# Performance work log

Measured on AMD Instinct MI355X. Metric: run time of the kernel, lower is better.

The kernel has to match this reference:

```python
import jax, jax.numpy as jnp
import numpy as np
import math

FEATURE_DIM = 1024
NUM_HEADS = 16
HEAD_SIZE = FEATURE_DIM // NUM_HEADS


def setup_inputs() -> dict:
    key = jax.random.key(0)
    ks = jax.random.split(key, 5)
    B, T, C = 4, 2048, FEATURE_DIM
    scale = 1.0 / math.sqrt(C)
    x = jax.random.normal(ks[0], (B, T, C), dtype=jnp.float32)
    # attention_proj: Linear(C, 3C) -> weight (3C, C), bias (3C,)
    W_qkv = jax.random.uniform(ks[1], (3 * C, C), jnp.float32, -scale, scale)
    b_qkv = jax.random.uniform(ks[2], (3 * C,), jnp.float32, -scale, scale)
    # final_proj: Linear(C, C)
    W_out = jax.random.uniform(ks[3], (C, C), jnp.float32, -scale, scale)
    b_out = jax.random.uniform(ks[4], (C,), jnp.float32, -scale, scale)
    return {"x": x, "W_qkv": W_qkv, "b_qkv": b_qkv, "W_out": W_out, "b_out": b_out}


def reference(x, W_qkv, b_qkv, W_out, b_out):
    B, T, C = x.shape
    H, hs = NUM_HEADS, HEAD_SIZE
    qkv = x @ W_qkv.T + b_qkv                     # (B, T, 3C)
    qkv = qkv.reshape(B, T, H, 3 * hs)            # per-head interleaved q|k|v
    q = qkv[..., :hs]                             # (B, T, H, hs)
    k = qkv[..., hs:2 * hs]
    v = qkv[..., 2 * hs:]
    att = jnp.einsum('bthd,bshd->bhts', q, k) / math.sqrt(hs)  # (B, H, T, T)
    att_prob = jax.nn.softmax(att, axis=-1)
    att_v = jnp.einsum('bhts,bshd->bthd', att_prob, v)         # (B, T, H, hs)
    att_v = att_v.reshape(B, T, C)
    return att_v @ W_out.T + b_out
```

## Files before the change

### kernel.cpp

```cpp
#include <hip/hip_runtime.h>
#include <hip/hip_bf16.h>


typedef unsigned short u16;
typedef short bf16x8 __attribute__((ext_vector_type(8)));
typedef float floatx4 __attribute__((ext_vector_type(4)));

#define BB 4
#define TT 2048
#define CC 1024
#define HH 16

#if __has_builtin(__builtin_amdgcn_exp2f)
#define EXP2(x) __builtin_amdgcn_exp2f(x)
#else
#define EXP2(x) exp2f(x)
#endif

__device__ __forceinline__ u16 f2bf(float f) {
    __hip_bfloat16 h = __float2bfloat16(f);
    u16 r; __builtin_memcpy(&r, &h, 2); return r;
}
__device__ __forceinline__ unsigned pkbf(float lo, float hi) {
    __hip_bfloat162 h2 = __float22bfloat162_rn(float2{lo, hi});
    unsigned r; __builtin_memcpy(&r, &h2, 4); return r;
}
__device__ __forceinline__ bf16x8 cvt8(const float* p) {
    floatx4 a = *(const floatx4*)p;
    floatx4 b = *(const floatx4*)(p + 4);
    bf16x8 r;
    r[0] = (short)f2bf(a[0]); r[1] = (short)f2bf(a[1]);
    r[2] = (short)f2bf(a[2]); r[3] = (short)f2bf(a[3]);
    r[4] = (short)f2bf(b[0]); r[5] = (short)f2bf(b[1]);
    r[6] = (short)f2bf(b[2]); r[7] = (short)f2bf(b[3]);
    return r;
}
__device__ __forceinline__ int sw8(int row, int slot) {
    return row * 64 + (((slot ^ (row & 7)) & 7) << 3);
}
__device__ __forceinline__ void gll16(const u16* g, u16* l) {
    __builtin_amdgcn_global_load_lds(
        (const __attribute__((address_space(1))) unsigned*)g,
        (__attribute__((address_space(3))) unsigned*)l, 16, 0, 0);
}

__device__ __forceinline__ void pl32swap(unsigned& a, unsigned& b) {
#if __has_builtin(__builtin_amdgcn_permlane32_swap)
    typedef unsigned u32x2 __attribute__((ext_vector_type(2)));
    u32x2 r = __builtin_amdgcn_permlane32_swap(a, b, false, false);
    a = r[0]; b = r[1];
#else
    const bool up = (threadIdx.x & 32) != 0;
    unsigned as = (unsigned)__shfl_xor((int)a, 32);
    unsigned bs = (unsigned)__shfl_xor((int)b, 32);
    unsigned na = up ? bs : a;
    unsigned nb = up ? b : as;
    a = na; b = nb;
#endif
}
__device__ __forceinline__ void pl16swap(unsigned& a, unsigned& b) {
#if __has_builtin(__builtin_amdgcn_permlane16_swap)
    typedef unsigned u32x2 __attribute__((ext_vector_type(2)));
    u32x2 r = __builtin_amdgcn_permlane16_swap(a, b, false, false);
    a = r[0]; b = r[1];
#else
    const bool up = (threadIdx.x & 16) != 0;
    unsigned as = (unsigned)__shfl_xor((int)a, 16);
    unsigned bs = (unsigned)__shfl_xor((int)b, 16);
    unsigned na = up ? bs : a;
    unsigned nb = up ? b : as;
    a = na; b = nb;
#endif
}

__global__ __launch_bounds__(256) void cvt_all(const float* __restrict__ x,
                                               const float* __restrict__ wq,
                                               const float* __restrict__ wo,
                                               u16* __restrict__ xb,
                                               u16* __restrict__ wqb,
                                               u16* __restrict__ wob) {
    const int nx8 = 8388608 / 8, nq8 = 3145728 / 8, no8 = 1048576 / 8;
    const int n8 = nx8 + nq8 + no8;
    for (int i = blockIdx.x * blockDim.x + threadIdx.x; i < n8;
         i += gridDim.x * blockDim.x) {
        const float* src;
        u16* dst;
        if (i < nx8)            { src = x  + (size_t)i * 8;          dst = xb  + (size_t)i * 8; }
        else if (i < nx8 + nq8) { size_t j = i - nx8; src = wq + j * 8; dst = wqb + j * 8; }
        else                    { size_t j = i - nx8 - nq8; src = wo + j * 8; dst = wob + j * 8; }
        floatx4 a = *(const floatx4*)src;
        floatx4 b = *(const floatx4*)(src + 4);
        union { bf16x8 v; unsigned u[4]; } r;
        r.u[0] = pkbf(a[0], a[1]); r.u[1] = pkbf(a[2], a[3]);
        r.u[2] = pkbf(b[0], b[1]); r.u[3] = pkbf(b[2], b[3]);
        *(bf16x8*)dst = r.v;
    }
}

template <int SCATTER, int QSLOT>
__global__ __launch_bounds__(256) void gemm_lds(const u16* __restrict__ Ab,
                                                const u16* __restrict__ Bb,
                                                const float* __restrict__ bias,
                                                void* __restrict__ Cv,
                                                int K, int N) {
    __shared__ u16 As[128 * 64];
    __shared__ u16 Bs[128 * 64];

    const int tid  = threadIdx.x;
    const int lane = tid & 63;
    const int wave = tid >> 6;
    const int quad = lane >> 4;
    const int l15  = lane & 15;
    const int wm   = (wave >> 1) * 64;
    const int wn   = (wave & 1) * 64;
    const int blockM = blockIdx.y * 128;
    const int blockN = blockIdx.x * 128;

    floatx4 acc[4][4];
#pragma unroll
    for (int i = 0; i < 4; i++)
#pragma unroll
        for (int j = 0; j < 4; j++) acc[i][j] = (floatx4){0.f, 0.f, 0.f, 0.f};

    const int lr = lane >> 3;
    const int scol = ((lane & 7) ^ (lr & 7)) * 8;

    for (int k0 = 0; k0 < K; k0 += 64) {
        __syncthreads();
#pragma unroll
        for (int i = 0; i < 4; i++) {
            const int c = wave * 4 + i;
            const int row = blockM + c * 8 + lr;
            const u16* src;
            if (QSLOT) {
                const int b = row >> 11, t = row & 2047, h = k0 >> 6;
                src = Ab + ((size_t)((b * HH + h) * TT + t)) * 192 + scol;
            } else {
                src = Ab + (size_t)row * K + k0 + scol;
            }
            gll16(src, &As[c * 512]);
        }
#pragma unroll
        for (int i = 0; i < 4; i++) {
            const int c = wave * 4 + i;
            const int row = blockN + c * 8 + lr;
            gll16(Bb + (size_t)row * K + k0 + scol, &Bs[c * 512]);
        }
        __syncthreads();

#pragma unroll
        for (int ks = 0; ks < 2; ks++) {
            const int slot = ks * 4 + quad;
            bf16x8 af[4], bfr[4];
#pragma unroll
            for (int mi = 0; mi < 4; mi++)
                af[mi] = *(const bf16x8*)&As[sw8(wm + mi * 16 + l15, slot)];
#pragma unroll
            for (int ni = 0; ni < 4; ni++)
                bfr[ni] = *(const bf16x8*)&Bs[sw8(wn + ni * 16 + l15, slot)];
#pragma unroll
            for (int mi = 0; mi < 4; mi++)
#pragma unroll
                for (int ni = 0; ni < 4; ni++)
                    acc[mi][ni] = __builtin_amdgcn_mfma_f32_16x16x32_bf16(
                        af[mi], bfr[ni], acc[mi][ni], 0, 0, 0);
        }
    }

#pragma unroll
    for (int ni = 0; ni < 4; ni++) {
        const int col = blockN + wn + ni * 16 + l15;
        const float bv = bias[col];
        if (SCATTER) {
            const int h = col / 192;
            const int r = col - h * 192;
            u16* C = (u16*)Cv;
#pragma unroll
            for (int mi = 0; mi < 4; mi++)
#pragma unroll
                for (int reg = 0; reg < 4; reg++) {
                    const int row = blockM + wm + mi * 16 + quad * 4 + reg;
                    const int b = row >> 11, t = row & 2047;
                    C[((size_t)((b * HH + h) * TT + t)) * 192 + r] =
                        f2bf(acc[mi][ni][reg] + bv);
                }
        } else {
            float* C = (float*)Cv;
#pragma unroll
            for (int mi = 0; mi < 4; mi++)
#pragma unroll
                for (int reg = 0; reg < 4; reg++) {
                    const int row = blockM + wm + mi * 16 + quad * 4 + reg;
                    C[(size_t)row * N + col] = acc[mi][ni][reg] + bv;
                }
        }
    }
}

template <int SCATTER, int QSLOT>
__global__ __launch_bounds__(256) void gemm_bt(const void* __restrict__ Av,
                                               const float* __restrict__ Bw,
                                               const float* __restrict__ bias,
                                               void* __restrict__ Cv,
                                               int K, int N) {
    __shared__ u16 As[128 * 64];
    __shared__ u16 Bs[128 * 64];

    const int tid  = threadIdx.x;
    const int lane = tid & 63;
    const int wave = tid >> 6;
    const int quad = lane >> 4;
    const int l15  = lane & 15;
    const int wm   = (wave >> 1) * 64;
    const int wn   = (wave & 1) * 64;
    const int blockM = blockIdx.y * 128;
    const int blockN = blockIdx.x * 128;

    floatx4 acc[4][4];
#pragma unroll
    for (int i = 0; i < 4; i++)
#pragma unroll
        for (int j = 0; j < 4; j++) acc[i][j] = (floatx4){0.f, 0.f, 0.f, 0.f};

    const int srow = lane >> 3;
    const int scol = (lane & 7) * 8;

    for (int k0 = 0; k0 < K; k0 += 64) {
        bf16x8 at[4], bt[4];
#pragma unroll
        for (int i = 0; i < 4; i++) {
            const int row = blockM + (i * 4 + wave) * 8 + srow;
            if (QSLOT) {
                const int b = row >> 11, t = row & 2047, h = k0 >> 6;
                at[i] = *(const bf16x8*)((const u16*)Av
                         + ((size_t)((b * HH + h) * TT + t)) * 192 + scol);
            } else {
                at[i] = cvt8((const float*)Av + (size_t)row * K + k0 + scol);
            }
        }
#pragma unroll
        for (int i = 0; i < 4; i++)
            bt[i] = cvt8(Bw + (size_t)(blockN + (i * 4 + wave) * 8 + srow) * K + k0 + scol);

        __syncthreads();
#pragma unroll
        for (int i = 0; i < 4; i++)
            *(bf16x8*)&As[sw8((i * 4 + wave) * 8 + srow, lane & 7)] = at[i];
#pragma unroll
        for (int i = 0; i < 4; i++)
            *(bf16x8*)&Bs[sw8((i * 4 + wave) * 8 + srow, lane & 7)] = bt[i];
        __syncthreads();

#pragma unroll
        for (int ks = 0; ks < 2; ks++) {
            const int slot = ks * 4 + quad;
            bf16x8 af[4], bfr[4];
#pragma unroll
            for (int mi = 0; mi < 4; mi++)
                af[mi] = *(const bf16x8*)&As[sw8(wm + mi * 16 + l15, slot)];
#pragma unroll
            for (int ni = 0; ni < 4; ni++)
                bfr[ni] = *(const bf16x8*)&Bs[sw8(wn + ni * 16 + l15, slot)];
#pragma unroll
            for (int mi = 0; mi < 4; mi++)
#pragma unroll
                for (int ni = 0; ni < 4; ni++)
                    acc[mi][ni] = __builtin_amdgcn_mfma_f32_16x16x32_bf16(
                        af[mi], bfr[ni], acc[mi][ni], 0, 0, 0);
        }
    }

#pragma unroll
    for (int ni = 0; ni < 4; ni++) {
        const int col = blockN + wn + ni * 16 + l15;
        const float bv = bias[col];
        if (SCATTER) {
            const int h = col / 192;
            const int r = col - h * 192;
            u16* C = (u16*)Cv;
#pragma unroll
            for (int mi = 0; mi < 4; mi++)
#pragma unroll
                for (int reg = 0; reg < 4; reg++) {
                    const int row = blockM + wm + mi * 16 + quad * 4 + reg;
                    const int b = row >> 11, t = row & 2047;
                    C[((size_t)((b * HH + h) * TT + t)) * 192 + r] =
                        f2bf(acc[mi][ni][reg] + bv);
                }
        } else {
            float* C = (float*)Cv;
#pragma unroll
            for (int mi = 0; mi < 4; mi++)
#pragma unroll
                for (int reg = 0; reg < 4; reg++) {
                    const int row = blockM + wm + mi * 16 + quad * 4 + reg;
                    C[(size_t)row * N + col] = acc[mi][ni][reg] + bv;
                }
        }
    }
}

__global__ __launch_bounds__(256) void attn_fwd(u16* __restrict__ qkv) {
    __shared__ u16 Ks[64 * 64];
    __shared__ u16 Vts[64 * 64];

    const int tid  = threadIdx.x;
    const int lane = tid & 63;
    const int wave = tid >> 6;
    const int quad = lane >> 4;
    const int l15  = lane & 15;

    const int bh = blockIdx.y;
    const int t0 = blockIdx.x * 128;
    u16* Qg = qkv + (size_t)bh * TT * 192;

    bf16x8 qf[2][2];
#pragma unroll
    for (int qi = 0; qi < 2; qi++) {
        const int trow = t0 + wave * 32 + qi * 16 + l15;
#pragma unroll
        for (int ks = 0; ks < 2; ks++)
            qf[qi][ks] = *(const bf16x8*)(Qg + (size_t)trow * 192 + ks * 32 + quad * 8);
    }

    floatx4 o[2][4];
#pragma unroll
    for (int qi = 0; qi < 2; qi++)
#pragma unroll
        for (int di = 0; di < 4; di++) o[qi][di] = (floatx4){0.f, 0.f, 0.f, 0.f};
    float l_run[2] = {0.f, 0.f};

    const float cexp = 0.18033688f;
    const int srow = lane >> 3;
    const int scol = (lane & 7) * 8;
    const int vs   = lane;
    const int vd0  = wave * 16;

    for (int s0 = 0; s0 < TT; s0 += 64) {
        bf16x8 kt[2];
#pragma unroll
        for (int i = 0; i < 2; i++)
            kt[i] = *(const bf16x8*)(Qg + (size_t)(s0 + (i * 4 + wave) * 8 + srow) * 192
                                     + 64 + scol);
        const u16* vp = Qg + (size_t)(s0 + vs) * 192 + 128 + vd0;
        bf16x8 v0 = *(const bf16x8*)vp;
        bf16x8 v1 = *(const bf16x8*)(vp + 8);

        __syncthreads();
#pragma unroll
        for (int i = 0; i < 2; i++)
            *(bf16x8*)&Ks[sw8((i * 4 + wave) * 8 + srow, lane & 7)] = kt[i];
        {
            const int vslot = vs >> 3, voff = vs & 7;
#pragma unroll
            for (int j = 0; j < 8; j++) {
                const int row = vd0 + j;
                Vts[row * 64 + (((vslot ^ (row & 7)) & 7) << 3) + voff] = (u16)v0[j];
            }
#pragma unroll
            for (int j = 0; j < 8; j++) {
                const int row = vd0 + 8 + j;
                Vts[row * 64 + (((vslot ^ (row & 7)) & 7) << 3) + voff] = (u16)v1[j];
            }
        }
        __syncthreads();

        floatx4 s_acc[4][2];
#pragma unroll
        for (int si = 0; si < 4; si++)
#pragma unroll
            for (int qi = 0; qi < 2; qi++) s_acc[si][qi] = (floatx4){0.f, 0.f, 0.f, 0.f};
#pragma unroll
        for (int ks = 0; ks < 2; ks++) {
            const int slot = ks * 4 + quad;
            bf16x8 kf[4];
#pragma unroll
            for (int si = 0; si < 4; si++)
                kf[si] = *(const bf16x8*)&Ks[sw8(si * 16 + l15, slot)];
#pragma unroll
            for (int si = 0; si < 4; si++)
#pragma unroll
                for (int qi = 0; qi < 2; qi++)
                    s_acc[si][qi] = __builtin_amdgcn_mfma_f32_16x16x32_bf16(
                        kf[si], qf[qi][ks], s_acc[si][qi], 0, 0, 0);
        }

        unsigned c[4][2][2];
        floatx4 rs[2] = {(floatx4){0.f,0.f,0.f,0.f}, (floatx4){0.f,0.f,0.f,0.f}};
#pragma unroll
        for (int si = 0; si < 4; si++)
#pragma unroll
            for (int qi = 0; qi < 2; qi++) {
                floatx4 p;
#pragma unroll
                for (int r = 0; r < 4; r++) p[r] = EXP2(s_acc[si][qi][r] * cexp);
                rs[qi] += p;
                c[si][qi][0] = pkbf(p[0], p[1]);
                c[si][qi][1] = pkbf(p[2], p[3]);
            }
#pragma unroll
        for (int qi = 0; qi < 2; qi++) {
            float v = rs[qi][0] + rs[qi][1] + rs[qi][2] + rs[qi][3];
            v += __shfl_xor(v, 16);
            v += __shfl_xor(v, 32);
            l_run[qi] += v;
        }

        union PF { bf16x8 v; unsigned u[4]; } pf[2][2];
#pragma unroll
        for (int qi = 0; qi < 2; qi++)
#pragma unroll
            for (int ks = 0; ks < 2; ks++)
#pragma unroll
                for (int h = 0; h < 2; h++) {
                    unsigned a = c[2 * ks][qi][h];
                    unsigned b = c[2 * ks + 1][qi][h];
                    pl32swap(a, b);
                    pl16swap(a, b);
                    pf[qi][ks].u[h]     = a;
                    pf[qi][ks].u[2 + h] = b;
                }

#pragma unroll
        for (int ks = 0; ks < 2; ks++) {
            const int slot = ks * 4 + quad;
            bf16x8 vf[4];
#pragma unroll
            for (int di = 0; di < 4; di++)
                vf[di] = *(const bf16x8*)&Vts[sw8(di * 16 + l15, slot)];
#pragma unroll
            for (int qi = 0; qi < 2; qi++)
#pragma unroll
                for (int di = 0; di < 4; di++)
                    o[qi][di] = __builtin_amdgcn_mfma_f32_16x16x32_bf16(
                        pf[qi][ks].v, vf[di], o[qi][di], 0, 0, 0);
        }
    }

#pragma unroll
    for (int qi = 0; qi < 2; qi++)
#pragma unroll
        for (int reg = 0; reg < 4; reg++) {
            const float lv = __shfl(l_run[qi], quad * 4 + reg);
            const float inv_l = 1.0f / lv;
            const int trow = t0 + wave * 32 + qi * 16 + quad * 4 + reg;
#pragma unroll
            for (int di = 0; di < 4; di++)
                Qg[(size_t)trow * 192 + di * 16 + l15] = f2bf(o[qi][di][reg] * inv_l);
        }
}

extern "C" void kernel_launch(void* const* d_in, const int* in_sizes, int n_in,
                              void* d_out, int out_size, void* d_ws, size_t ws_size,
                              hipStream_t stream) {
    (void)out_size;
    float* out = (float*)d_out;

    const float *x = nullptr, *wq = nullptr, *bq = nullptr, *wo = nullptr, *bo = nullptr;
    int found = 0;
    for (int i = 0; i < n_in && i < 8; i++) {
        switch (in_sizes[i]) {
            case 8388608: x  = (const float*)d_in[i]; found |= 1;  break;
            case 3145728: wq = (const float*)d_in[i]; found |= 2;  break;
            case 3072:    bq = (const float*)d_in[i]; found |= 4;  break;
            case 1048576: wo = (const float*)d_in[i]; found |= 8;  break;
            case 1024:    bo = (const float*)d_in[i]; found |= 16; break;
        }
    }
    if (found != 31) {
        x  = (const float*)d_in[0]; wq = (const float*)d_in[1];
        bq = (const float*)d_in[2]; wo = (const float*)d_in[3];
        bo = (const float*)d_in[4];
    }

    u16* qkv = (u16*)d_ws;

    if (ws_size >= 75497472u) {
        u16* xb  = qkv + 25165824;
        u16* wqb = qkv + 33554432;
        u16* wob = qkv + 36700160;

        cvt_all<<<2048, 256, 0, stream>>>(x, wq, wo, xb, wqb, wob);
        gemm_lds<1, 0><<<dim3(3 * CC / 128, BB * TT / 128), 256, 0, stream>>>(
            xb, wqb, bq, qkv, CC, 3 * CC);
        attn_fwd<<<dim3(TT / 128, BB * HH), 256, 0, stream>>>(qkv);
        gemm_lds<0, 1><<<dim3(CC / 128, BB * TT / 128), 256, 0, stream>>>(
            qkv, wob, bo, out, CC, CC);
    } else {
        gemm_bt<1, 0><<<dim3(3 * CC / 128, BB * TT / 128), 256, 0, stream>>>(
            x, wq, bq, qkv, CC, 3 * CC);
        attn_fwd<<<dim3(TT / 128, BB * HH), 256, 0, stream>>>(qkv);
        gemm_bt<0, 1><<<dim3(CC / 128, BB * TT / 128), 256, 0, stream>>>(
            qkv, wo, bo, out, CC, CC);
    }
}
```

Before: 304.6 us.

## Pre-transpose V into separate buffer, load K/V via direct-to-LDS, remap GEMM tiles

Adds a transpose_v kernel that writes V in a (bh, d, t) layout so the attention kernel can fill its K and V LDS tiles with direct global-to-LDS 16-byte loads. This replaces the per-element scattered transposing stores into LDS. The GEMM kernels also remap workgroup IDs in groups of 8 so that neighbouring workgroups are spread across the grid, intended to improve cache locality across XCDs. The cost is one extra kernel launch and an extra read and write of V, plus a larger workspace requirement, with the old path kept as a fallback.

Result: slower. 330.8 us (+8.6%).

```diff
diff --git a/kernel.cpp b/kernel.cpp
--- a/kernel.cpp
+++ b/kernel.cpp
@@ -97,6 +97,41 @@
     }
 }
 
+__global__ __launch_bounds__(256) void transpose_v(const u16* __restrict__ qkv,
+                                                   u16* __restrict__ Vt) {
+    __shared__ u16 L[128 * 64];
+    const int tid = threadIdx.x;
+    const int bh  = blockIdx.y;
+    const int t0  = blockIdx.x * 128;
+    const u16* Vg = qkv + (size_t)bh * TT * 192 + 128;
+
+    const int lr = tid >> 3;
+    const int p8 = tid & 7;
+#pragma unroll
+    for (int p = 0; p < 4; p++) {
+        const int t = p * 32 + lr;
+        bf16x8 v = *(const bf16x8*)(Vg + (size_t)(t0 + t) * 192 + p8 * 8);
+        *(bf16x8*)&L[sw8(t, p8)] = v;
+    }
+    __syncthreads();
+
+    const int tseg = (tid & 15) * 8;
+    const int dq   = tid >> 4;
+#pragma unroll
+    for (int p = 0; p < 4; p++) {
+        const int d = p * 16 + dq;
+        const int slot = d >> 3, off = d & 7;
+        union { bf16x8 v; u16 e[8]; } r;
+#pragma unroll
+        for (int j = 0; j < 8; j++) {
+            const int jj = (j + tid) & 7;
+            const int t = tseg + jj;
+            r.e[jj] = L[t * 64 + (((slot ^ (t & 7)) & 7) << 3) + off];
+        }
+        *(bf16x8*)(Vt + ((size_t)bh * 64 + d) * TT + t0 + tseg) = r.v;
+    }
+}
+
 template <int SCATTER, int QSLOT>
 __global__ __launch_bounds__(256) void gemm_lds(const u16* __restrict__ Ab,
                                                 const u16* __restrict__ Bb,
@@ -113,8 +148,12 @@
     const int l15  = lane & 15;
     const int wm   = (wave >> 1) * 64;
     const int wn   = (wave & 1) * 64;
-    const int blockM = blockIdx.y * 128;
-    const int blockN = blockIdx.x * 128;
+
+    const int gx = gridDim.x, nwg = gx * gridDim.y;
+    int id = blockIdx.y * gx + blockIdx.x;
+    if ((nwg & 7) == 0) id = (id & 7) * (nwg >> 3) + (id >> 3);
+    const int blockM = (id / gx) * 128;
+    const int blockN = (id % gx) * 128;
 
     floatx4 acc[4][4];
 #pragma unroll
@@ -300,7 +339,9 @@
     }
 }
 
-__global__ __launch_bounds__(256) void attn_fwd(u16* __restrict__ qkv) {
+template <int VT>
+__global__ __launch_bounds__(256) void attn_fwd(u16* __restrict__ qkv,
+                                                const u16* __restrict__ Vt) {
     __shared__ u16 Ks[64 * 64];
     __shared__ u16 Vts[64 * 64];
 
@@ -313,6 +354,7 @@
     const int bh = blockIdx.y;
     const int t0 = blockIdx.x * 128;
     u16* Qg = qkv + (size_t)bh * TT * 192;
+    const u16* VtB = Vt + (size_t)bh * 64 * TT;
 
     bf16x8 qf[2][2];
 #pragma unroll
@@ -331,39 +373,57 @@
     float l_run[2] = {0.f, 0.f};
 
     const float cexp = 0.18033688f;
-    const int srow = lane >> 3;
-    const int scol = (lane & 7) * 8;
+    const int lr   = lane >> 3;
+    const int scolsw = ((lane & 7) ^ (lr & 7)) * 8;
+    const int scol   = (lane & 7) * 8;
     const int vs   = lane;
     const int vd0  = wave * 16;
 
     for (int s0 = 0; s0 < TT; s0 += 64) {
-        bf16x8 kt[2];
-#pragma unroll
-        for (int i = 0; i < 2; i++)
-            kt[i] = *(const bf16x8*)(Qg + (size_t)(s0 + (i * 4 + wave) * 8 + srow) * 192
-                                     + 64 + scol);
-        const u16* vp = Qg + (size_t)(s0 + vs) * 192 + 128 + vd0;
-        bf16x8 v0 = *(const bf16x8*)vp;
-        bf16x8 v1 = *(const bf16x8*)(vp + 8);
-
-        __syncthreads();
-#pragma unroll
-        for (int i = 0; i < 2; i++)
-            *(bf16x8*)&Ks[sw8((i * 4 + wave) * 8 + srow, lane & 7)] = kt[i];
-        {
-            const int vslot = vs >> 3, voff = vs & 7;
-#pragma unroll
-            for (int j = 0; j < 8; j++) {
-                const int row = vd0 + j;
-                Vts[row * 64 + (((vslot ^ (row & 7)) & 7) << 3) + voff] = (u16)v0[j];
+        if (VT) {
+            __syncthreads();
+#pragma unroll
+            for (int i = 0; i < 2; i++) {
+                const int c = wave * 2 + i;
+                gll16(Qg + (size_t)(s0 + c * 8 + lr) * 192 + 64 + scolsw,
+                      &Ks[c * 512]);
             }
 #pragma unroll
-            for (int j = 0; j < 8; j++) {
-                const int row = vd0 + 8 + j;
-                Vts[row * 64 + (((vslot ^ (row & 7)) & 7) << 3) + voff] = (u16)v1[j];
+            for (int i = 0; i < 2; i++) {
+                const int c = wave * 2 + i;
+                gll16(VtB + (size_t)(c * 8 + lr) * TT + s0 + scolsw,
+                      &Vts[c * 512]);
             }
-        }
-        __syncthreads();
+            __syncthreads();
+        } else {
+            bf16x8 kt[2];
+#pragma unroll
+            for (int i = 0; i < 2; i++)
+                kt[i] = *(const bf16x8*)(Qg + (size_t)(s0 + (i * 4 + wave) * 8 + lr) * 192
+                                         + 64 + scol);
+            const u16* vp = Qg + (size_t)(s0 + vs) * 192 + 128 + vd0;
+            bf16x8 v0 = *(const bf16x8*)vp;
+            bf16x8 v1 = *(const bf16x8*)(vp + 8);
+
+            __syncthreads();
+#pragma unroll
+            for (int i = 0; i < 2; i++)
+                *(bf16x8*)&Ks[sw8((i * 4 + wave) * 8 + lr, lane & 7)] = kt[i];
+            {
+                const int vslot = vs >> 3, voff = vs & 7;
+#pragma unroll
+                for (int j = 0; j < 8; j++) {
+                    const int row = vd0 + j;
+                    Vts[row * 64 + (((vslot ^ (row & 7)) & 7) << 3) + voff] = (u16)v0[j];
+                }
+#pragma unroll
+                for (int j = 0; j < 8; j++) {
+                    const int row = vd0 + 8 + j;
+                    Vts[row * 64 + (((vslot ^ (row & 7)) & 7) << 3) + voff] = (u16)v1[j];
+                }
+            }
+            __syncthreads();
+        }
 
         floatx4 s_acc[4][2];
 #pragma unroll
@@ -475,22 +535,31 @@
 
     u16* qkv = (u16*)d_ws;
 
-    if (ws_size >= 75497472u) {
+    const dim3 g1(3 * CC / 128, BB * TT / 128), ga(TT / 128, BB * HH),
+               g3(CC / 128, BB * TT / 128);
+
+    if (ws_size >= 92274688u) {
         u16* xb  = qkv + 25165824;
         u16* wqb = qkv + 33554432;
         u16* wob = qkv + 36700160;
+        u16* Vt  = qkv + 37748736;
 
         cvt_all<<<2048, 256, 0, stream>>>(x, wq, wo, xb, wqb, wob);
-        gemm_lds<1, 0><<<dim3(3 * CC / 128, BB * TT / 128), 256, 0, stream>>>(
-            xb, wqb, bq, qkv, CC, 3 * CC);
-        attn_fwd<<<dim3(TT / 128, BB * HH), 256, 0, stream>>>(qkv);
-        gemm_lds<0, 1><<<dim3(CC / 128, BB * TT / 128), 256, 0, stream>>>(
-            qkv, wob, bo, out, CC, CC);
+        gemm_lds<1, 0><<<g1, 256, 0, stream>>>(xb, wqb, bq, qkv, CC, 3 * CC);
+        transpose_v<<<ga, 256, 0, stream>>>(qkv, Vt);
+        attn_fwd<1><<<ga, 256, 0, stream>>>(qkv, Vt);
+        gemm_lds<0, 1><<<g3, 256, 0, stream>>>(qkv, wob, bo, out, CC, CC);
+    } else if (ws_size >= 75497472u) {
+        u16* xb  = qkv + 25165824;
+        u16* wqb = qkv + 33554432;
+        u16* wob = qkv + 36700160;
+        cvt_all<<<2048, 256, 0, stream>>>(x, wq, wo, xb, wqb, wob);
+        gemm_lds<1, 0><<<g1, 256, 0, stream>>>(xb, wqb, bq, qkv, CC, 3 * CC);
+        attn_fwd<0><<<ga, 256, 0, stream>>>(qkv, nullptr);
+        gemm_lds<0, 1><<<g3, 256, 0, stream>>>(qkv, wob, bo, out, CC, CC);
     } else {
-        gemm_bt<1, 0><<<dim3(3 * CC / 128, BB * TT / 128), 256, 0, stream>>>(
-            x, wq, bq, qkv, CC, 3 * CC);
-        attn_fwd<<<dim3(TT / 128, BB * HH), 256, 0, stream>>>(qkv);
-        gemm_bt<0, 1><<<dim3(CC / 128, BB * TT / 128), 256, 0, stream>>>(
-            qkv, wo, bo, out, CC, CC);
-    }
-}
+        gemm_bt<1, 0><<<g1, 256, 0, stream>>>(x, wq, bq, qkv, CC, 3 * CC);
+        attn_fwd<0><<<ga, 256, 0, stream>>>(qkv, nullptr);
+        gemm_bt<0, 1><<<g3, 256, 0, stream>>>(qkv, wo, bo, out, CC, CC);
+    }
+}
```

## Fold softmax scale into Q, compute row sums via MFMA, async-load K to LDS

Applied to the files above, without the earlier changes.

The QKV GEMM epilogue now premultiplies Q columns by the log2-scaled softmax factor, so the attention loop drops the per-element multiply before exp2. The softmax row sum is accumulated with an extra MFMA against a vector of bf16 ones instead of VALU adds and cross-lane shuffles. K tiles are loaded with a direct global-to-LDS instruction (gll16) with pre-swizzled addresses instead of going through registers. In exchange, row sums are now taken from bf16-rounded probabilities, and Q is stored in bf16 after scaling, which slightly changes rounding. The kernel still runs without a running max.

Result: faster. 295.0 us (-3.2%).

```diff
diff --git a/kernel.cpp b/kernel.cpp
--- a/kernel.cpp
+++ b/kernel.cpp
@@ -10,6 +10,7 @@
 #define TT 2048
 #define CC 1024
 #define HH 16
+#define CEXP 0.18033688f
 
 #if __has_builtin(__builtin_amdgcn_exp2f)
 #define EXP2(x) __builtin_amdgcn_exp2f(x)
@@ -174,6 +175,7 @@
         if (SCATTER) {
             const int h = col / 192;
             const int r = col - h * 192;
+            const float qs = (r < 64) ? CEXP : 1.0f;
             u16* C = (u16*)Cv;
 #pragma unroll
             for (int mi = 0; mi < 4; mi++)
@@ -182,7 +184,7 @@
                     const int row = blockM + wm + mi * 16 + quad * 4 + reg;
                     const int b = row >> 11, t = row & 2047;
                     C[((size_t)((b * HH + h) * TT + t)) * 192 + r] =
-                        f2bf(acc[mi][ni][reg] + bv);
+                        f2bf((acc[mi][ni][reg] + bv) * qs);
                 }
         } else {
             float* C = (float*)Cv;
@@ -277,6 +279,7 @@
         if (SCATTER) {
             const int h = col / 192;
             const int r = col - h * 192;
+            const float qs = (r < 64) ? CEXP : 1.0f;
             u16* C = (u16*)Cv;
 #pragma unroll
             for (int mi = 0; mi < 4; mi++)
@@ -285,7 +288,7 @@
                     const int row = blockM + wm + mi * 16 + quad * 4 + reg;
                     const int b = row >> 11, t = row & 2047;
                     C[((size_t)((b * HH + h) * TT + t)) * 192 + r] =
-                        f2bf(acc[mi][ni][reg] + bv);
+                        f2bf((acc[mi][ni][reg] + bv) * qs);
                 }
         } else {
             float* C = (float*)Cv;
@@ -323,33 +326,33 @@
             qf[qi][ks] = *(const bf16x8*)(Qg + (size_t)trow * 192 + ks * 32 + quad * 8);
     }
 
+    bf16x8 ones;
+#pragma unroll
+    for (int j = 0; j < 8; j++) ones[j] = (short)0x3F80;
+
     floatx4 o[2][4];
 #pragma unroll
     for (int qi = 0; qi < 2; qi++)
 #pragma unroll
         for (int di = 0; di < 4; di++) o[qi][di] = (floatx4){0.f, 0.f, 0.f, 0.f};
-    float l_run[2] = {0.f, 0.f};
-
-    const float cexp = 0.18033688f;
-    const int srow = lane >> 3;
-    const int scol = (lane & 7) * 8;
+    floatx4 l_acc[2] = {(floatx4){0.f,0.f,0.f,0.f}, (floatx4){0.f,0.f,0.f,0.f}};
+
+    const int lr = lane >> 3;
+    const int scolsw = ((lane & 7) ^ (lr & 7)) * 8;
     const int vs   = lane;
     const int vd0  = wave * 16;
 
     for (int s0 = 0; s0 < TT; s0 += 64) {
-        bf16x8 kt[2];
-#pragma unroll
-        for (int i = 0; i < 2; i++)
-            kt[i] = *(const bf16x8*)(Qg + (size_t)(s0 + (i * 4 + wave) * 8 + srow) * 192
-                                     + 64 + scol);
         const u16* vp = Qg + (size_t)(s0 + vs) * 192 + 128 + vd0;
         bf16x8 v0 = *(const bf16x8*)vp;
         bf16x8 v1 = *(const bf16x8*)(vp + 8);
 
         __syncthreads();
 #pragma unroll
-        for (int i = 0; i < 2; i++)
-            *(bf16x8*)&Ks[sw8((i * 4 + wave) * 8 + srow, lane & 7)] = kt[i];
+        for (int i = 0; i < 2; i++) {
+            const int c = wave * 2 + i;
+            gll16(Qg + (size_t)(s0 + c * 8 + lr) * 192 + 64 + scolsw, &Ks[c * 512]);
+        }
         {
             const int vslot = vs >> 3, voff = vs & 7;
 #pragma unroll
@@ -386,25 +389,16 @@
         }
 
         unsigned c[4][2][2];
-        floatx4 rs[2] = {(floatx4){0.f,0.f,0.f,0.f}, (floatx4){0.f,0.f,0.f,0.f}};
 #pragma unroll
         for (int si = 0; si < 4; si++)
 #pragma unroll
             for (int qi = 0; qi < 2; qi++) {
                 floatx4 p;
 #pragma unroll
-                for (int r = 0; r < 4; r++) p[r] = EXP2(s_acc[si][qi][r] * cexp);
-                rs[qi] += p;
+                for (int r = 0; r < 4; r++) p[r] = EXP2(s_acc[si][qi][r]);
                 c[si][qi][0] = pkbf(p[0], p[1]);
                 c[si][qi][1] = pkbf(p[2], p[3]);
             }
-#pragma unroll
-        for (int qi = 0; qi < 2; qi++) {
-            float v = rs[qi][0] + rs[qi][1] + rs[qi][2] + rs[qi][3];
-            v += __shfl_xor(v, 16);
-            v += __shfl_xor(v, 32);
-            l_run[qi] += v;
-        }
 
         union PF { bf16x8 v; unsigned u[4]; } pf[2][2];
 #pragma unroll
@@ -429,11 +423,14 @@
             for (int di = 0; di < 4; di++)
                 vf[di] = *(const bf16x8*)&Vts[sw8(di * 16 + l15, slot)];
 #pragma unroll
-            for (int qi = 0; qi < 2; qi++)
+            for (int qi = 0; qi < 2; qi++) {
 #pragma unroll
                 for (int di = 0; di < 4; di++)
                     o[qi][di] = __builtin_amdgcn_mfma_f32_16x16x32_bf16(
                         pf[qi][ks].v, vf[di], o[qi][di], 0, 0, 0);
+                l_acc[qi] = __builtin_amdgcn_mfma_f32_16x16x32_bf16(
+                    pf[qi][ks].v, ones, l_acc[qi], 0, 0, 0);
+            }
         }
     }
 
@@ -441,8 +438,7 @@
     for (int qi = 0; qi < 2; qi++)
 #pragma unroll
         for (int reg = 0; reg < 4; reg++) {
-            const float lv = __shfl(l_run[qi], quad * 4 + reg);
-            const float inv_l = 1.0f / lv;
+            const float inv_l = 1.0f / l_acc[qi][reg];
             const int trow = t0 + wave * 32 + qi * 16 + quad * 4 + reg;
 #pragma unroll
             for (int di = 0; di < 4; di++)
@@ -475,22 +471,20 @@
 
     u16* qkv = (u16*)d_ws;
 
+    const dim3 g1(3 * CC / 128, BB * TT / 128), ga(TT / 128, BB * HH),
+               g3(CC / 128, BB * TT / 128);
+
     if (ws_size >= 75497472u) {
         u16* xb  = qkv + 25165824;
         u16* wqb = qkv + 33554432;
         u16* wob = qkv + 36700160;
-
         cvt_all<<<2048, 256, 0, stream>>>(x, wq, wo, xb, wqb, wob);
-        gemm_lds<1, 0><<<dim3(3 * CC / 128, BB * TT / 128), 256, 0, stream>>>(
-            xb, wqb, bq, qkv, CC, 3 * CC);
-        attn_fwd<<<dim3(TT / 128, BB * HH), 256, 0, stream>>>(qkv);
-        gemm_lds<0, 1><<<dim3(CC / 128, BB * TT / 128), 256, 0, stream>>>(
-            qkv, wob, bo, out, CC, CC);
+        gemm_lds<1, 0><<<g1, 256, 0, stream>>>(xb, wqb, bq, qkv, CC, 3 * CC);
+        attn_fwd<<<ga, 256, 0, stream>>>(qkv);
+        gemm_lds<0, 1><<<g3, 256, 0, stream>>>(qkv, wob, bo, out, CC, CC);
     } else {
-        gemm_bt<1, 0><<<dim3(3 * CC / 128, BB * TT / 128), 256, 0, stream>>>(
-            x, wq, bq, qkv, CC, 3 * CC);
-        attn_fwd<<<dim3(TT / 128, BB * HH), 256, 0, stream>>>(qkv);
-        gemm_bt<0, 1><<<dim3(CC / 128, BB * TT / 128), 256, 0, stream>>>(
-            qkv, wo, bo, out, CC, CC);
-    }
-}
+        gemm_bt<1, 0><<<g1, 256, 0, stream>>>(x, wq, bq, qkv, CC, 3 * CC);
+        attn_fwd<<<ga, 256, 0, stream>>>(qkv);
+        gemm_bt<0, 1><<<g3, 256, 0, stream>>>(qkv, wo, bo, out, CC, CC);
+    }
+}
```
